# Kernel optimization log

Measured on AMD Instinct MI355X. Metric: run time of the kernel, lower is better.

## Reference

```python
import jax, jax.numpy as jnp
import numpy as np

B, M, N = 4, 1024, 4096
DQ, DC, H, DH = 512, 512, 8, 64
D = H * DH
NEG = -10000000.0


def setup_inputs() -> dict:
    key = jax.random.key(0)
    ks = jax.random.split(key, 7)
    left = jax.random.normal(ks[0], (B, M, DQ), dtype=jnp.float32)
    right = jax.random.normal(ks[1], (B, N, DC), dtype=jnp.float32)
    mask = jax.random.randint(ks[2], (B, M, N), 0, 2).astype(bool)
    # learned params (torch Linear stores weight as (out,in); we store (in,out))
    Wq = jax.random.normal(ks[3], (DQ, D), dtype=jnp.float32) * (DQ ** -0.5)
    Wkv = jax.random.normal(ks[4], (DC, 2 * D), dtype=jnp.float32) * (DC ** -0.5)
    Wout = jax.random.normal(ks[5], (D, DQ), dtype=jnp.float32) * (D ** -0.5)
    bout = jax.random.normal(ks[6], (DQ,), dtype=jnp.float32) * 0.01
    return {"left": left, "right": right, "mask": mask,
            "Wq": Wq, "Wkv": Wkv, "Wout": Wout, "bout": bout}


def reference(left, right, mask, Wq, Wkv, Wout, bout):
    scale = DH ** -0.5
    q = left @ Wq                      # (B, M, D)
    kv = right @ Wkv                   # (B, N, 2D)
    k, v = jnp.split(kv, 2, axis=-1)   # (B, N, D) each
    q = q.reshape(B, M, H, DH).transpose(0, 2, 1, 3)  # (B, H, M, DH)
    k = k.reshape(B, N, H, DH).transpose(0, 2, 1, 3)  # (B, H, N, DH)
    v = v.reshape(B, N, H, DH).transpose(0, 2, 1, 3)  # (B, H, N, DH)
    sim = scale * jnp.einsum('bhmd,bhnd->bhmn', q, k)  # (B, H, M, N)
    sim = jnp.where(mask[:, None, :, :], sim, NEG)
    attn = jax.nn.softmax(sim, axis=-1)
    out = jnp.einsum('bhmn,bhnd->bhmd', attn, v)       # (B, H, M, DH)
    out = out.transpose(0, 2, 1, 3).reshape(B, M, D)
    return out @ Wout + bout           # (B, M, DQ)
```

## Files before the change

kernel.cpp:

```cpp
#include <hip/hip_runtime.h>

typedef _Float16 f16;
typedef __attribute__((ext_vector_type(8))) _Float16 half8;
typedef __attribute__((ext_vector_type(4))) _Float16 half4;
typedef __attribute__((ext_vector_type(4))) float floatx4;
typedef unsigned int uint32;
typedef __attribute__((ext_vector_type(4))) uint32 uint4v;

#define MFMA16(a, b, c) __builtin_amdgcn_mfma_f32_16x16x32_f16((a), (b), (c), 0, 0, 0)

constexpr int B_ = 4, M_ = 1024, N_ = 4096, DQ_ = 512, DC_ = 512, H_ = 8, DH_ = 64, D_ = 512;
constexpr int KP_ = 576;
constexpr int VP_ = 4224;
constexpr int NSPLIT = 4;
constexpr float QSC_ = 0.18033688011112042f;

typedef __attribute__((address_space(1))) const void glds_g;
typedef __attribute__((address_space(3))) void glds_l;
__device__ __forceinline__ void g2lds16(const void* g, void* l) {
    __builtin_amdgcn_global_load_lds((glds_g*)g, (glds_l*)l, 16, 0, 0);
}

__device__ __forceinline__ void wtr_tile(const float* __restrict__ src, f16* __restrict__ dst,
                                         int Nout, int bx, int by, int tid) {
    __shared__ __align__(16) f16 Ts[64][72];
    const int n0 = bx * 64, k0 = by * 64;
    {
        int kr = tid >> 2, q4 = tid & 3;
        const float* sp = src + (size_t)(k0 + kr) * Nout + n0 + q4 * 16;
        float4 x0 = *(const float4*)(sp + 0), x1 = *(const float4*)(sp + 4);
        float4 x2 = *(const float4*)(sp + 8), x3 = *(const float4*)(sp + 12);
        half8 h0, h1;
        h0[0]=(f16)x0.x; h0[1]=(f16)x0.y; h0[2]=(f16)x0.z; h0[3]=(f16)x0.w;
        h0[4]=(f16)x1.x; h0[5]=(f16)x1.y; h0[6]=(f16)x1.z; h0[7]=(f16)x1.w;
        h1[0]=(f16)x2.x; h1[1]=(f16)x2.y; h1[2]=(f16)x2.z; h1[3]=(f16)x2.w;
        h1[4]=(f16)x3.x; h1[5]=(f16)x3.y; h1[6]=(f16)x3.z; h1[7]=(f16)x3.w;
        *(half8*)&Ts[kr][q4 * 16] = h0;
        *(half8*)&Ts[kr][q4 * 16 + 8] = h1;
    }
    __syncthreads();
    {
        int nr = tid >> 2, q = tid & 3;
        half8 h0, h1;
#pragma unroll
        for (int j = 0; j < 8; j++) { h0[j] = Ts[q * 16 + j][nr]; h1[j] = Ts[q * 16 + 8 + j][nr]; }
        f16* dp = dst + (size_t)(n0 + nr) * 512 + k0 + q * 16;
        *(half8*)(dp + 0) = h0;
        *(half8*)(dp + 8) = h1;
    }
}

__global__ __launch_bounds__(256)
void prep_k(const void* __restrict__ mask, uint32* __restrict__ bits,
            const float* __restrict__ left, f16* __restrict__ leftb,
            const float* __restrict__ right, f16* __restrict__ rightb,
            const float* __restrict__ Wq, f16* __restrict__ wqt,
            const float* __restrict__ Wkv, f16* __restrict__ wkvt,
            const float* __restrict__ Wout, f16* __restrict__ woutt) {
    const int blk = blockIdx.x, tid = threadIdx.x;
    if (blk < 4096) {
        __shared__ int s_bad;
        if (tid == 0) s_bad = 0;
        __syncthreads();
        const uint32* w = (const uint32*)mask + (size_t)blk * 1024;
        int bad = 0;
#pragma unroll
        for (int j = 0; j < 4; j++) bad |= (w[tid * 4 + j] & 0xFFFFFFFEu) != 0u;
        if (bad) s_bad = 1;
        __syncthreads();
        const bool bytes_mode = s_bad != 0;
        const size_t base = (size_t)blk * 4096;
        const int lane = tid & 63;
        for (int j = 0; j < 16; j++) {
            size_t e = base + j * 256 + tid;
            bool pred = bytes_mode ? (((const unsigned char*)mask)[e] != 0)
                                   : (((const int*)mask)[e] != 0);
            unsigned long long bal = __ballot(pred);
            if (lane == 0)       bits[e >> 5] = (uint32)bal;
            else if (lane == 32) bits[e >> 5] = (uint32)(bal >> 32);
        }
    } else if (blk < 6144) {
        int i = ((blk - 4096) * 256 + tid) * 4;
        float4 x = *(const float4*)(left + i);
        half4 h; h[0] = (f16)x.x; h[1] = (f16)x.y; h[2] = (f16)x.z; h[3] = (f16)x.w;
        *(half4*)(leftb + i) = h;
    } else if (blk < 14336) {
        int i = ((blk - 6144) * 256 + tid) * 4;
        float4 x = *(const float4*)(right + i);
        half4 h; h[0] = (f16)x.x; h[1] = (f16)x.y; h[2] = (f16)x.z; h[3] = (f16)x.w;
        *(half4*)(rightb + i) = h;
    } else if (blk < 14400) {
        int r = blk - 14336;
        wtr_tile(Wq, wqt, 512, r & 7, r >> 3, tid);
    } else if (blk < 14528) {
        int r = blk - 14400;
        wtr_tile(Wkv, wkvt, 1024, r & 15, r >> 4, tid);
    } else {
        int r = blk - 14528;
        wtr_tile(Wout, woutt, 512, r & 7, r >> 3, tid);
    }
}

__global__ __launch_bounds__(256)
void gemmqkv_k(const f16* __restrict__ leftb, const f16* __restrict__ wqt,
               const f16* __restrict__ rightb, const f16* __restrict__ wkvt,
               f16* __restrict__ qb, f16* __restrict__ kb, f16* __restrict__ vt) {
    __shared__ __align__(16) f16 As[2][128 * 64];
    __shared__ __align__(16) f16 Bs[2][128 * 64];
    const int blk = blockIdx.x, tid = threadIdx.x;
    const int lane = tid & 63, wave = tid >> 6;
    const int qd = lane >> 4, l16 = lane & 15;
    const int wm = wave >> 1, wn = wave & 1;

    int mode;
    const f16* A; const f16* Bt; size_t m0, n0;
    if (blk < 1024) {
        size_t rows = (size_t)(blk & 127) * 128, cols = (size_t)(blk >> 7) * 128;
        if (cols < 512) { mode = 0; A = rightb; m0 = rows; Bt = wkvt;   n0 = cols; }
        else            { mode = 1; A = wkvt;   m0 = cols; Bt = rightb; n0 = rows; }
    } else {
        int r = blk - 1024;
        mode = 2; A = leftb; Bt = wqt;
        m0 = (size_t)(r & 31) * 128; n0 = (size_t)(r >> 5) * 128;
    }

    size_t goff[4];
    f16 *la[2][4], *lb[2][4];
#pragma unroll
    for (int i = 0; i < 4; i++) {
        int c = i * 256 + wave * 64 + lane;
        int row = c >> 3, col8 = (c & 7) ^ (row & 7);
        goff[i] = (size_t)row * 512 + col8 * 8;
        la[0][i] = &As[0][(size_t)(i * 256 + wave * 64) * 8];
        la[1][i] = &As[1][(size_t)(i * 256 + wave * 64) * 8];
        lb[0][i] = &Bs[0][(size_t)(i * 256 + wave * 64) * 8];
        lb[1][i] = &Bs[1][(size_t)(i * 256 + wave * 64) * 8];
    }
    const f16* Ab = A + m0 * 512;
    const f16* Bb = Bt + n0 * 512;

    floatx4 acc[4][4] = {};

#pragma unroll
    for (int i = 0; i < 4; i++) g2lds16(Ab + goff[i], la[0][i]);
#pragma unroll
    for (int i = 0; i < 4; i++) g2lds16(Bb + goff[i], lb[0][i]);
    int cur = 0;

    for (int k0 = 0; k0 < 512; k0 += 64) {
        __syncthreads();
        if (k0 + 64 < 512) {
            const int nxt = cur ^ 1;
#pragma unroll
            for (int i = 0; i < 4; i++) g2lds16(Ab + goff[i] + k0 + 64, la[nxt][i]);
#pragma unroll
            for (int i = 0; i < 4; i++) g2lds16(Bb + goff[i] + k0 + 64, lb[nxt][i]);
        }
        const f16* Ac = &As[cur][0];
        const f16* Bc = &Bs[cur][0];
#pragma unroll
        for (int kk = 0; kk < 2; kk++) {
            half8 a[4], b[4];
#pragma unroll
            for (int t = 0; t < 4; t++) {
                int rowa = wm * 64 + t * 16 + l16;
                int rowb = wn * 64 + t * 16 + l16;
                int pa8 = ((kk * 4 + qd) ^ (rowa & 7)) * 8;
                int pb8 = ((kk * 4 + qd) ^ (rowb & 7)) * 8;
                a[t] = *(const half8*)&Ac[rowa * 64 + pa8];
                b[t] = *(const half8*)&Bc[rowb * 64 + pb8];
            }
#pragma unroll
            for (int mt = 0; mt < 4; mt++)
#pragma unroll
                for (int nt = 0; nt < 4; nt++)
                    acc[mt][nt] = MFMA16(a[mt], b[nt], acc[mt][nt]);
        }
        cur ^= 1;
    }

#pragma unroll
    for (int mt = 0; mt < 4; mt++)
#pragma unroll
        for (int nt = 0; nt < 4; nt++)
#pragma unroll
            for (int r = 0; r < 4; r++) {
                size_t mi = m0 + wm * 64 + mt * 16 + qd * 4 + r;
                size_t ni = n0 + wn * 64 + nt * 16 + l16;
                float v = acc[mt][nt][r];
                if (mode == 2) {
                    qb[mi * 512 + ni] = (f16)v;
                } else if (mode == 0) {
                    kb[mi * KP_ + ni] = (f16)v;
                } else {
                    int dcol = (int)mi - 512;
                    int hh = dcol >> 6, dh = dcol & 63;
                    size_t bb = ni >> 12, nn = ni & 4095;
                    vt[((bb * H_ + hh) * (size_t)DH_ + dh) * VP_ + nn] = (f16)v;
                }
            }
}

__global__ __launch_bounds__(512, 8)
void attn_k(const f16* __restrict__ Qb, const f16* __restrict__ Kb,
            const f16* __restrict__ Vt, const uint32* __restrict__ mb,
            float* __restrict__ Op, float* __restrict__ Lp) {
    const int tid = threadIdx.x;
    const int lane = tid & 63, wave = tid >> 6;
    const int qd = lane >> 4, l16 = lane & 15;
    const int bh = blockIdx.x, b = bh >> 3, h = bh & 7;
    const int z = blockIdx.z;
    constexpr int iters = N_ / (64 * NSPLIT);
    const int n_base = z * iters * 64;
    const int m_base = blockIdx.y * 128 + wave * 16;

    __shared__ __align__(16) f16 Ks[2][64 * 64];
    __shared__ __align__(16) f16 Vs[2][64 * 64];

    half8 q0, q1;
    {
        const f16* qrow = Qb + ((size_t)(b * M_ + m_base + l16)) * D_ + h * DH_;
        half8 r0 = *(const half8*)(qrow + qd * 8);
        half8 r1 = *(const half8*)(qrow + 32 + qd * 8);
#pragma unroll
        for (int j = 0; j < 8; j++) {
            q0[j] = (f16)((float)r0[j] * QSC_);
            q1[j] = (f16)((float)r1[j] * QSC_);
        }
    }

    floatx4 ot[4] = {};
    float l_acc = 0.0f;

    const uint32* mrow = mb + ((size_t)(b * M_ + m_base + l16)) * (N_ / 32);

    const int srow = wave * 8;
    const int r8 = lane >> 3, p8 = lane & 7;
    const int gc8 = p8 ^ r8;
    const f16* kg = Kb + ((size_t)(b * N_) + srow + r8) * KP_ + h * DH_ + gc8 * 8;
    const f16* vg = Vt + ((size_t)(bh * DH_) + srow + r8) * VP_ + gc8 * 8;

    auto stage = [&](int buf, int n0) {
        g2lds16(kg + (size_t)n0 * KP_, &Ks[buf][srow * 64]);
        g2lds16(vg + n0, &Vs[buf][srow * 64]);
    };

    stage(0, n_base);
    uint2 mmc = *(const uint2*)(mrow + (n_base >> 5));
    int cur = 0;

    const int swz = (l16 & 7);

    for (int it = 0; it < iters; it++) {
        const int n0 = n_base + it * 64;
        __syncthreads();
        uint2 mmn;
        if (it + 1 < iters) {
            stage(cur ^ 1, n0 + 64);
            mmn = *(const uint2*)(mrow + ((n0 + 64) >> 5));
        }

        const uint32 u0 = mmc.x >> (qd * 4);
        const uint32 u1 = mmc.y >> (qd * 4);

        uint32 pk[4][2];
#pragma unroll
        for (int s = 0; s < 4; s++) {
            const int ro = (s * 16 + l16) * 64;
            half8 k0 = *(const half8*)&Ks[cur][ro + ((qd ^ swz) * 8)];
            half8 k1 = *(const half8*)&Ks[cur][ro + (((4 + qd) ^ swz) * 8)];
            floatx4 t = {};
            t = MFMA16(k0, q0, t);
            t = MFMA16(k1, q1, t);
            uint32 us = (s & 2 ? u1 : u0) >> ((s & 1) * 16);
            float e0 = __builtin_amdgcn_exp2f(t[0]);
            float e1 = __builtin_amdgcn_exp2f(t[1]);
            float e2 = __builtin_amdgcn_exp2f(t[2]);
            float e3 = __builtin_amdgcn_exp2f(t[3]);
            e0 = (us & 1u) ? e0 : 0.0f;
            e1 = (us & 2u) ? e1 : 0.0f;
            e2 = (us & 4u) ? e2 : 0.0f;
            e3 = (us & 8u) ? e3 : 0.0f;
            l_acc += (e0 + e1) + (e2 + e3);
            pk[s][0] = __builtin_bit_cast(uint32, __builtin_amdgcn_cvt_pkrtz(e0, e1));
            pk[s][1] = __builtin_bit_cast(uint32, __builtin_amdgcn_cvt_pkrtz(e2, e3));
        }

        half8 pa[2];
#pragma unroll
        for (int hh = 0; hh < 2; hh++) {
            uint32 w0, w1, w2, w3;
            {
                auto a = __builtin_amdgcn_permlane32_swap(pk[2 * hh][0], pk[2 * hh + 1][0], false, false);
                auto c = __builtin_amdgcn_permlane16_swap(a[0], a[1], false, false);
                w0 = c[0]; w2 = c[1];
            }
            {
                auto a = __builtin_amdgcn_permlane32_swap(pk[2 * hh][1], pk[2 * hh + 1][1], false, false);
                auto c = __builtin_amdgcn_permlane16_swap(a[0], a[1], false, false);
                w1 = c[0]; w3 = c[1];
            }
            uint4v wv = {w0, w1, w2, w3};
            pa[hh] = __builtin_bit_cast(half8, wv);
        }

#pragma unroll
        for (int sd = 0; sd < 4; sd++) {
            const int ro = (sd * 16 + l16) * 64;
            half8 v0 = *(const half8*)&Vs[cur][ro + ((qd ^ swz) * 8)];
            half8 v1 = *(const half8*)&Vs[cur][ro + (((4 + qd) ^ swz) * 8)];
            ot[sd] = MFMA16(v0, pa[0], ot[sd]);
            ot[sd] = MFMA16(v1, pa[1], ot[sd]);
        }
        mmc = mmn;
        cur ^= 1;
    }

    l_acc += __shfl_xor(l_acc, 16);
    l_acc += __shfl_xor(l_acc, 32);

    {
        size_t row = (size_t)(z * 32 + bh) * M_ + m_base + l16;
        float* op = Op + row * DH_ + qd * 4;
#pragma unroll
        for (int sd = 0; sd < 4; sd++)
            __builtin_nontemporal_store(ot[sd], (floatx4*)(op + sd * 16));
        if (qd == 0) __builtin_nontemporal_store(l_acc, Lp + row);
    }
}

__global__ __launch_bounds__(256)
void comb_k(const float* __restrict__ Op, const float* __restrict__ Lp, f16* __restrict__ Ob,
            int nsp) {
    int i = blockIdx.x * 256 + threadIdx.x;
    int d4 = i & 15, m = (i >> 4) & 1023, bh = i >> 14;
    float nx = 0.f, ny = 0.f, nz = 0.f, nw = 0.f, den = 0.f;
    for (int s = 0; s < nsp; s++) {
        size_t row = ((size_t)s * 32 + bh) * M_ + m;
        float4 x = *(const float4*)(Op + row * DH_ + d4 * 4);
        nx += x.x; ny += x.y; nz += x.z; nw += x.w;
        den += Lp[row];
    }
    float r = 1.0f / den;
    int b = bh >> 3, h = bh & 7;
    f16* o = Ob + ((size_t)(b * M_ + m)) * D_ + h * DH_ + d4 * 4;
    half4 hv; hv[0] = (f16)(nx * r); hv[1] = (f16)(ny * r); hv[2] = (f16)(nz * r); hv[3] = (f16)(nw * r);
    *(half4*)o = hv;
}

__global__ __launch_bounds__(256)
void gemmout_k(const f16* __restrict__ A, const f16* __restrict__ Bt,
               float* __restrict__ Fout, const float* __restrict__ bias) {
    __shared__ __align__(16) f16 As[2][64 * 64];
    __shared__ __align__(16) f16 Bs[2][64 * 64];
    const int tid = threadIdx.x;
    const int lane = tid & 63, wave = tid >> 6;
    const int qd = lane >> 4, l16 = lane & 15;
    const int wm = wave >> 1, wn = wave & 1;
    const size_t m0 = (size_t)blockIdx.x * 64;
    const size_t n0 = (size_t)blockIdx.y * 64;

    size_t goff[2];
    f16 *la[2][2], *lb[2][2];
#pragma unroll
    for (int i = 0; i < 2; i++) {
        int c = i * 256 + wave * 64 + lane;
        int row = c >> 3, col8 = (c & 7) ^ (row & 7);
        goff[i] = (size_t)row * 512 + col8 * 8;
        la[0][i] = &As[0][(size_t)(i * 256 + wave * 64) * 8];
        la[1][i] = &As[1][(size_t)(i * 256 + wave * 64) * 8];
        lb[0][i] = &Bs[0][(size_t)(i * 256 + wave * 64) * 8];
        lb[1][i] = &Bs[1][(size_t)(i * 256 + wave * 64) * 8];
    }
    const f16* Ab = A + m0 * 512;
    const f16* Bb = Bt + n0 * 512;

    floatx4 acc[2][2] = {};

#pragma unroll
    for (int i = 0; i < 2; i++) g2lds16(Ab + goff[i], la[0][i]);
#pragma unroll
    for (int i = 0; i < 2; i++) g2lds16(Bb + goff[i], lb[0][i]);
    int cur = 0;

    for (int k0 = 0; k0 < 512; k0 += 64) {
        __syncthreads();
        if (k0 + 64 < 512) {
            const int nxt = cur ^ 1;
#pragma unroll
            for (int i = 0; i < 2; i++) g2lds16(Ab + goff[i] + k0 + 64, la[nxt][i]);
#pragma unroll
            for (int i = 0; i < 2; i++) g2lds16(Bb + goff[i] + k0 + 64, lb[nxt][i]);
        }
        const f16* Ac = &As[cur][0];
        const f16* Bc = &Bs[cur][0];
#pragma unroll
        for (int kk = 0; kk < 2; kk++) {
            half8 a[2], b[2];
#pragma unroll
            for (int t = 0; t < 2; t++) {
                int rowa = wm * 32 + t * 16 + l16;
                int rowb = wn * 32 + t * 16 + l16;
                int pa8 = ((kk * 4 + qd) ^ (rowa & 7)) * 8;
                int pb8 = ((kk * 4 + qd) ^ (rowb & 7)) * 8;
                a[t] = *(const half8*)&Ac[rowa * 64 + pa8];
                b[t] = *(const half8*)&Bc[rowb * 64 + pb8];
            }
#pragma unroll
            for (int mt = 0; mt < 2; mt++)
#pragma unroll
                for (int nt = 0; nt < 2; nt++)
                    acc[mt][nt] = MFMA16(a[mt], b[nt], acc[mt][nt]);
        }
        cur ^= 1;
    }

#pragma unroll
    for (int mt = 0; mt < 2; mt++)
#pragma unroll
        for (int nt = 0; nt < 2; nt++)
#pragma unroll
            for (int r = 0; r < 4; r++) {
                size_t row = m0 + wm * 32 + mt * 16 + qd * 4 + r;
                size_t col = n0 + wn * 32 + nt * 16 + l16;
                Fout[row * 512 + col] = acc[mt][nt][r] + bias[col];
            }
}

extern "C" void kernel_launch(void* const* d_in, const int* in_sizes, int n_in,
                              void* d_out, int out_size, void* d_ws, size_t ws_size,
                              hipStream_t stream) {
    const float* left  = (const float*)d_in[0];
    const float* right = (const float*)d_in[1];
    const void*  mask  = d_in[2];
    const float* Wq    = (const float*)d_in[3];
    const float* Wkv   = (const float*)d_in[4];
    const float* Wout  = (const float*)d_in[5];
    const float* bout  = (const float*)d_in[6];

    char* ws = (char*)d_ws;
    size_t off = 0;
    auto take = [&](size_t bytes) { char* p = ws + off; off += (bytes + 255) & ~(size_t)255; return p; };
    uint32* mbits = (uint32*)take((size_t)B_ * M_ * N_ / 8);
    f16* woutt = (f16*)take((size_t)D_ * DQ_ * 2);
    f16* qb    = (f16*)take((size_t)B_ * M_ * D_ * 2);
    f16* kb    = (f16*)take((size_t)B_ * N_ * KP_ * 2);
    f16* vt    = (f16*)take((size_t)B_ * H_ * DH_ * VP_ * 2);
    f16* ob    = (f16*)take((size_t)B_ * M_ * D_ * 2);
    char* pool = (char*)take((size_t)34 * 1024 * 1024);
    f16* leftb  = (f16*)pool;
    f16* rightb = (f16*)(pool + (size_t)4 * 1024 * 1024);
    f16* wqt    = (f16*)(pool + (size_t)20 * 1024 * 1024);
    f16* wkvt   = (f16*)(pool + (size_t)21 * 1024 * 1024);
    float* Op   = (float*)pool;
    float* Lp   = (float*)(pool + (size_t)NSPLIT * 32 * M_ * DH_ * 4);

    prep_k<<<14592, 256, 0, stream>>>(mask, mbits, left, leftb, right, rightb,
                                      Wq, wqt, Wkv, wkvt, Wout, woutt);
    gemmqkv_k<<<1152, 256, 0, stream>>>(leftb, wqt, rightb, wkvt, qb, kb, vt);
    attn_k<<<dim3(32, 8, NSPLIT), 512, 0, stream>>>(qb, kb, vt, mbits, Op, Lp);
    comb_k<<<2048, 256, 0, stream>>>(Op, Lp, ob, NSPLIT);
    gemmout_k<<<dim3(64, 8), 256, 0, stream>>>(ob, woutt, (float*)d_out, bout);
}
```

Baseline: 271.0 us.

## Vectorize mask packing, remap GEMM tiles per XCD, single-buffer LDS, prefetch K/V fragments

The mask-to-bits pass now loads 16 mask elements per thread with vector loads and packs them with shifts plus one shuffle, replacing a per-element ballot loop. The QKV GEMM remaps block indices so that each XCD handles a contiguous group of row tiles, which should improve L2 reuse. It also drops LDS double buffering in favour of a single buffer with two barriers per k-step, which halves LDS use but exposes global load latency. In the attention loop, K and V fragments are software-prefetched one sub-tile ahead so LDS reads overlap the MFMAs.

```diff
diff --git a/kernel.cpp b/kernel.cpp
--- a/kernel.cpp
+++ b/kernel.cpp
@@ -69,16 +69,26 @@
         if (bad) s_bad = 1;
         __syncthreads();
         const bool bytes_mode = s_bad != 0;
-        const size_t base = (size_t)blk * 4096;
-        const int lane = tid & 63;
-        for (int j = 0; j < 16; j++) {
-            size_t e = base + j * 256 + tid;
-            bool pred = bytes_mode ? (((const unsigned char*)mask)[e] != 0)
-                                   : (((const int*)mask)[e] != 0);
-            unsigned long long bal = __ballot(pred);
-            if (lane == 0)       bits[e >> 5] = (uint32)bal;
-            else if (lane == 32) bits[e >> 5] = (uint32)(bal >> 32);
-        }
+        uint32 v = 0;
+        if (bytes_mode) {
+            uint4 x = *(const uint4*)((const unsigned char*)mask + (size_t)blk * 4096 + tid * 16);
+            uint32 ws_[4] = {x.x, x.y, x.z, x.w};
+#pragma unroll
+            for (int k = 0; k < 4; k++)
+#pragma unroll
+                for (int bb = 0; bb < 4; bb++)
+                    v |= (((ws_[k] >> (8 * bb)) & 0xFFu) != 0u ? 1u : 0u) << (k * 4 + bb);
+        } else {
+            const uint4* p = (const uint4*)((const uint32*)mask + (size_t)blk * 4096 + tid * 16);
+            uint4 x0 = p[0], x1 = p[1], x2 = p[2], x3 = p[3];
+            uint32 ws_[16] = {x0.x, x0.y, x0.z, x0.w, x1.x, x1.y, x1.z, x1.w,
+                              x2.x, x2.y, x2.z, x2.w, x3.x, x3.y, x3.z, x3.w};
+#pragma unroll
+            for (int k = 0; k < 16; k++) v |= (ws_[k] != 0u ? 1u : 0u) << k;
+        }
+        uint32 other = (uint32)__shfl_xor((int)v, 1);
+        if ((tid & 1) == 0)
+            bits[(size_t)blk * 128 + (tid >> 1)] = v | (other << 16);
     } else if (blk < 6144) {
         int i = ((blk - 4096) * 256 + tid) * 4;
         float4 x = *(const float4*)(left + i);
@@ -105,59 +115,53 @@
 void gemmqkv_k(const f16* __restrict__ leftb, const f16* __restrict__ wqt,
                const f16* __restrict__ rightb, const f16* __restrict__ wkvt,
                f16* __restrict__ qb, f16* __restrict__ kb, f16* __restrict__ vt) {
-    __shared__ __align__(16) f16 As[2][128 * 64];
-    __shared__ __align__(16) f16 Bs[2][128 * 64];
-    const int blk = blockIdx.x, tid = threadIdx.x;
+    __shared__ __align__(16) f16 As[128 * 64];
+    __shared__ __align__(16) f16 Bs[128 * 64];
+    const int hw = blockIdx.x, tid = threadIdx.x;
     const int lane = tid & 63, wave = tid >> 6;
     const int qd = lane >> 4, l16 = lane & 15;
     const int wm = wave >> 1, wn = wave & 1;
 
     int mode;
     const f16* A; const f16* Bt; size_t m0, n0;
-    if (blk < 1024) {
-        size_t rows = (size_t)(blk & 127) * 128, cols = (size_t)(blk >> 7) * 128;
+    if (hw < 1024) {
+        const int xcd = hw & 7, slot = hw >> 3;
+        const int mi_ = xcd * 16 + (slot & 15);
+        const int ni_ = slot >> 4;
+        size_t rows = (size_t)mi_ * 128, cols = (size_t)ni_ * 128;
         if (cols < 512) { mode = 0; A = rightb; m0 = rows; Bt = wkvt;   n0 = cols; }
         else            { mode = 1; A = wkvt;   m0 = cols; Bt = rightb; n0 = rows; }
     } else {
-        int r = blk - 1024;
+        const int r = hw - 1024;
+        const int xcd = r & 7, slot = r >> 3;
+        const int mi_ = xcd * 4 + (slot & 3);
+        const int ni_ = slot >> 2;
         mode = 2; A = leftb; Bt = wqt;
-        m0 = (size_t)(r & 31) * 128; n0 = (size_t)(r >> 5) * 128;
+        m0 = (size_t)mi_ * 128; n0 = (size_t)ni_ * 128;
     }
 
     size_t goff[4];
-    f16 *la[2][4], *lb[2][4];
+    f16 *la[4], *lb[4];
 #pragma unroll
     for (int i = 0; i < 4; i++) {
         int c = i * 256 + wave * 64 + lane;
         int row = c >> 3, col8 = (c & 7) ^ (row & 7);
         goff[i] = (size_t)row * 512 + col8 * 8;
-        la[0][i] = &As[0][(size_t)(i * 256 + wave * 64) * 8];
-        la[1][i] = &As[1][(size_t)(i * 256 + wave * 64) * 8];
-        lb[0][i] = &Bs[0][(size_t)(i * 256 + wave * 64) * 8];
-        lb[1][i] = &Bs[1][(size_t)(i * 256 + wave * 64) * 8];
+        la[i] = As + (size_t)(i * 256 + wave * 64) * 8;
+        lb[i] = Bs + (size_t)(i * 256 + wave * 64) * 8;
     }
     const f16* Ab = A + m0 * 512;
     const f16* Bb = Bt + n0 * 512;
 
     floatx4 acc[4][4] = {};
 
-#pragma unroll
-    for (int i = 0; i < 4; i++) g2lds16(Ab + goff[i], la[0][i]);
-#pragma unroll
-    for (int i = 0; i < 4; i++) g2lds16(Bb + goff[i], lb[0][i]);
-    int cur = 0;
-
     for (int k0 = 0; k0 < 512; k0 += 64) {
         __syncthreads();
-        if (k0 + 64 < 512) {
-            const int nxt = cur ^ 1;
-#pragma unroll
-            for (int i = 0; i < 4; i++) g2lds16(Ab + goff[i] + k0 + 64, la[nxt][i]);
-#pragma unroll
-            for (int i = 0; i < 4; i++) g2lds16(Bb + goff[i] + k0 + 64, lb[nxt][i]);
-        }
-        const f16* Ac = &As[cur][0];
-        const f16* Bc = &Bs[cur][0];
+#pragma unroll
+        for (int i = 0; i < 4; i++) g2lds16(Ab + goff[i] + k0, la[i]);
+#pragma unroll
+        for (int i = 0; i < 4; i++) g2lds16(Bb + goff[i] + k0, lb[i]);
+        __syncthreads();
 #pragma unroll
         for (int kk = 0; kk < 2; kk++) {
             half8 a[4], b[4];
@@ -167,8 +171,8 @@
                 int rowb = wn * 64 + t * 16 + l16;
                 int pa8 = ((kk * 4 + qd) ^ (rowa & 7)) * 8;
                 int pb8 = ((kk * 4 + qd) ^ (rowb & 7)) * 8;
-                a[t] = *(const half8*)&Ac[rowa * 64 + pa8];
-                b[t] = *(const half8*)&Bc[rowb * 64 + pb8];
+                a[t] = *(const half8*)&As[rowa * 64 + pa8];
+                b[t] = *(const half8*)&Bs[rowb * 64 + pb8];
             }
 #pragma unroll
             for (int mt = 0; mt < 4; mt++)
@@ -176,7 +180,6 @@
                 for (int nt = 0; nt < 4; nt++)
                     acc[mt][nt] = MFMA16(a[mt], b[nt], acc[mt][nt]);
         }
-        cur ^= 1;
     }
 
 #pragma unroll
@@ -250,6 +253,8 @@
     int cur = 0;
 
     const int swz = (l16 & 7);
+    const int c0 = (qd ^ swz) * 8;
+    const int c1 = ((4 + qd) ^ swz) * 8;
 
     for (int it = 0; it < iters; it++) {
         const int n0 = n_base + it * 64;
@@ -259,19 +264,25 @@
             stage(cur ^ 1, n0 + 64);
             mmn = *(const uint2*)(mrow + ((n0 + 64) >> 5));
         }
+        const f16* Kc = &Ks[cur][0];
+        const f16* Vc = &Vs[cur][0];
 
         const uint32 u0 = mmc.x >> (qd * 4);
         const uint32 u1 = mmc.y >> (qd * 4);
 
         uint32 pk[4][2];
+        half8 kc0 = *(const half8*)&Kc[(l16) * 64 + c0];
+        half8 kc1 = *(const half8*)&Kc[(l16) * 64 + c1];
 #pragma unroll
         for (int s = 0; s < 4; s++) {
-            const int ro = (s * 16 + l16) * 64;
-            half8 k0 = *(const half8*)&Ks[cur][ro + ((qd ^ swz) * 8)];
-            half8 k1 = *(const half8*)&Ks[cur][ro + (((4 + qd) ^ swz) * 8)];
             floatx4 t = {};
-            t = MFMA16(k0, q0, t);
-            t = MFMA16(k1, q1, t);
+            t = MFMA16(kc0, q0, t);
+            t = MFMA16(kc1, q1, t);
+            if (s < 3) {
+                const int ro = ((s + 1) * 16 + l16) * 64;
+                kc0 = *(const half8*)&Kc[ro + c0];
+                kc1 = *(const half8*)&Kc[ro + c1];
+            }
             uint32 us = (s & 2 ? u1 : u0) >> ((s & 1) * 16);
             float e0 = __builtin_amdgcn_exp2f(t[0]);
             float e1 = __builtin_amdgcn_exp2f(t[1]);
@@ -304,13 +315,19 @@
             pa[hh] = __builtin_bit_cast(half8, wv);
         }
 
+        half8 vc0 = *(const half8*)&Vc[(l16) * 64 + c0];
+        half8 vc1 = *(const half8*)&Vc[(l16) * 64 + c1];
 #pragma unroll
         for (int sd = 0; sd < 4; sd++) {
-            const int ro = (sd * 16 + l16) * 64;
-            half8 v0 = *(const half8*)&Vs[cur][ro + ((qd ^ swz) * 8)];
-            half8 v1 = *(const half8*)&Vs[cur][ro + (((4 + qd) ^ swz) * 8)];
-            ot[sd] = MFMA16(v0, pa[0], ot[sd]);
-            ot[sd] = MFMA16(v1, pa[1], ot[sd]);
+            floatx4 o = ot[sd];
+            o = MFMA16(vc0, pa[0], o);
+            o = MFMA16(vc1, pa[1], o);
+            if (sd < 3) {
+                const int ro = ((sd + 1) * 16 + l16) * 64;
+                vc0 = *(const half8*)&Vc[ro + c0];
+                vc1 = *(const half8*)&Vc[ro + c1];
+            }
+            ot[sd] = o;
         }
         mmc = mmn;
         cur ^= 1;
```

Measured after the change: 274.9 us. No clear change (+1.4%).
